# Optimization experiments

Hardware: AMD Instinct MI355X
Metric: run time of the kernel (lower is better)

## Reference

```python
import jax, jax.numpy as jnp
import numpy as np

HID = 1024
HEADS = 16
HEAD_DIM = HID // HEADS
SCALE = HEAD_DIM ** -0.5


def setup_inputs() -> dict:
    key = jax.random.key(0)
    ks = jax.random.split(key, 11)
    B, S = 4, 2048
    std = HID ** -0.5
    inp = {
        'q': jax.random.normal(ks[0], (B, S, HID), jnp.float32),
        'k': jax.random.normal(ks[1], (B, S, HID), jnp.float32),
        'v': jax.random.normal(ks[2], (B, S, HID), jnp.float32),
        'Wq': jax.random.normal(ks[3], (HID, HID), jnp.float32) * std,
        'bq': jnp.zeros((HID,), jnp.float32),
        'Wk': jax.random.normal(ks[4], (HID, HID), jnp.float32) * std,
        'bk': jnp.zeros((HID,), jnp.float32),
        'Wv': jax.random.normal(ks[5], (HID, HID), jnp.float32) * std,
        'bv': jnp.zeros((HID,), jnp.float32),
        'Wo': jax.random.normal(ks[6], (HID, HID), jnp.float32) * std,
        'bo': jnp.zeros((HID,), jnp.float32),
    }
    return inp


def _split_heads(x, B):
    # [B, S, HID] -> [B, H, S, Dh]
    return x.reshape(B, -1, HEADS, HEAD_DIM).transpose(0, 2, 1, 3)


def reference(q, k, v, Wq, bq, Wk, bk, Wv, bv, Wo, bo):
    B = q.shape[0]
    Q = _split_heads(jnp.dot(q, Wq.T) + bq, B)
    K = _split_heads(jnp.dot(k, Wk.T) + bk, B)
    V = _split_heads(jnp.dot(v, Wv.T) + bv, B)
    # [B, H, Sq, Sk]
    energy = jnp.einsum('bhqd,bhkd->bhqk', Q, K) * SCALE
    attention = jax.nn.softmax(energy, axis=-1)
    x = jnp.einsum('bhqk,bhkd->bhqd', attention, V)  # dropout = identity (eval)
    x = x.transpose(0, 2, 1, 3).reshape(B, -1, HID)
    x = jnp.dot(x, Wo.T) + bo
    return (x, attention)
```

## Files before the change

kernel.cpp:

```cpp
#include <hip/hip_runtime.h>
#include <stdint.h>

#define HID 1024
#define HEADS 16
#define HDIM 64
#define SEQ 2048
#define BATCH 4
#define SCALE 0.125f
#define EXPC 0.18033688011112042f

typedef __bf16 bf16x8 __attribute__((ext_vector_type(8)));
typedef float f32x4 __attribute__((ext_vector_type(4)));
typedef unsigned short ushortx8 __attribute__((ext_vector_type(8)));
typedef unsigned short ushortx4 __attribute__((ext_vector_type(4)));

__device__ __forceinline__ unsigned short f2bf(float f) {
  uint32_t u = __builtin_bit_cast(uint32_t, f);
  u = (u + 0x7fffu + ((u >> 16) & 1u)) >> 16;
  return (unsigned short)u;
}
__device__ __forceinline__ float bf2f(unsigned short u) {
  uint32_t x = ((uint32_t)u) << 16;
  return __builtin_bit_cast(float, x);
}
__device__ __forceinline__ void gl16(const void* g, void* l) {
  __builtin_amdgcn_global_load_lds(
      (const __attribute__((address_space(1))) unsigned int*)g,
      (__attribute__((address_space(3))) unsigned int*)l, 16, 0, 0);
}

struct ConvArgs {
  const float* s[7];
  unsigned short* d[7];
  int n[7];
};
__global__ __launch_bounds__(256) void convk(ConvArgs a) {
  const int ten = blockIdx.y;
  const float* s = a.s[ten];
  unsigned short* d = a.d[ten];
  const int n = a.n[ten];
  const int stride = gridDim.x * blockDim.x * 8;
  for (int i = (blockIdx.x * blockDim.x + threadIdx.x) * 8; i < n; i += stride) {
    float4 v0 = *(const float4*)(s + i);
    float4 v1 = *(const float4*)(s + i + 4);
    ushortx8 o = {f2bf(v0.x), f2bf(v0.y), f2bf(v0.z), f2bf(v0.w),
                  f2bf(v1.x), f2bf(v1.y), f2bf(v1.z), f2bf(v1.w)};
    *(ushortx8*)(d + i) = o;
  }
}

struct QkvArgs {
  const unsigned short* A[3];
  const unsigned short* W[3];
  const float* bias[3];
  unsigned short* out[3];
};
__global__ __launch_bounds__(256) void gemm_qkv(QkvArgs ar) {
  __shared__ unsigned short Als[128 * 64];
  __shared__ unsigned short Bls[128 * 64];
  const int z = blockIdx.z;
  const unsigned short* A = ar.A[z];
  const unsigned short* Wb = ar.W[z];
  const float* bias = ar.bias[z];
  unsigned short* Out = ar.out[z];

  const int t = threadIdx.x;
  const int bn = blockIdx.x, bm = blockIdx.y;
  const int w = t >> 6, lane = t & 63;
  const int wm = w >> 1, wn = w & 1;
  const int lr = lane & 15, lk = lane >> 4;
  const int row0 = bm * 128, col0 = bn * 128;

  const unsigned short* Abase =
      A + (size_t)(row0 + w * 32 + (lane >> 3)) * HID + (lane & 7) * 8;
  const unsigned short* Wbase =
      Wb + (size_t)(col0 + w * 32 + (lane >> 3)) * HID + (lane & 7) * 8;

  f32x4 acc[4][4] = {};

  for (int ks = 0; ks < 16; ++ks) {
    __syncthreads();
#pragma unroll
    for (int i = 0; i < 4; ++i)
      gl16(Abase + (size_t)i * 8 * HID + ks * 64, &Als[(w * 32 + i * 8) * 64]);
#pragma unroll
    for (int i = 0; i < 4; ++i)
      gl16(Wbase + (size_t)i * 8 * HID + ks * 64, &Bls[(w * 32 + i * 8) * 64]);
    __syncthreads();
#pragma unroll
    for (int kk = 0; kk < 2; ++kk) {
      bf16x8 a[4], bb[4];
#pragma unroll
      for (int f = 0; f < 4; ++f) {
        a[f] = *(const bf16x8*)&Als[(wm * 64 + f * 16 + lr) * 64 + kk * 32 + lk * 8];
        bb[f] = *(const bf16x8*)&Bls[(wn * 64 + f * 16 + lr) * 64 + kk * 32 + lk * 8];
      }
#pragma unroll
      for (int fm = 0; fm < 4; ++fm)
#pragma unroll
        for (int fn = 0; fn < 4; ++fn)
          acc[fm][fn] = __builtin_amdgcn_mfma_f32_16x16x32_bf16(
              a[fm], bb[fn], acc[fm][fn], 0, 0, 0);
    }
  }

#pragma unroll
  for (int fn = 0; fn < 4; ++fn) {
    int col = col0 + wn * 64 + fn * 16 + lr;
    float bv = bias[col];
#pragma unroll
    for (int fm = 0; fm < 4; ++fm) {
      int row = row0 + wm * 64 + fm * 16 + lk * 4;
      if (z == 2) {
        int b_ = row >> 11, s = row & 2047;
        int hh = col >> 6, d = col & 63;
        ushortx4 o4 = {f2bf(acc[fm][fn][0] + bv), f2bf(acc[fm][fn][1] + bv),
                       f2bf(acc[fm][fn][2] + bv), f2bf(acc[fm][fn][3] + bv)};
        *(ushortx4*)(Out + ((size_t)(b_ * HEADS + hh) * HDIM + d) * SEQ + s) = o4;
      } else {
#pragma unroll
        for (int r = 0; r < 4; ++r)
          Out[(size_t)(row + r) * HID + col] = f2bf(acc[fm][fn][r] + bv);
      }
    }
  }
}

template <int W_F32>
__global__ __launch_bounds__(256) void gemm_wo(
    const unsigned short* __restrict__ A, const void* __restrict__ Wp,
    const float* __restrict__ bias, float* __restrict__ Out) {
  __shared__ unsigned short Als[128 * 64];
  __shared__ unsigned short Bls[128 * 64];
  const int t = threadIdx.x;
  const int bn = blockIdx.x, bm = blockIdx.y;
  const int w = t >> 6, lane = t & 63;
  const int wm = w >> 1, wn = w & 1;
  const int lr = lane & 15, lk = lane >> 4;
  const int row0 = bm * 128, col0 = bn * 128;

  const unsigned short* Abase =
      A + (size_t)(row0 + w * 32 + (lane >> 3)) * HID + (lane & 7) * 8;
  const unsigned short* Wb16 =
      (const unsigned short*)Wp + (size_t)(col0 + w * 32 + (lane >> 3)) * HID +
      (lane & 7) * 8;

  f32x4 acc[4][4] = {};

  for (int ks = 0; ks < 16; ++ks) {
    __syncthreads();
#pragma unroll
    for (int i = 0; i < 4; ++i)
      gl16(Abase + (size_t)i * 8 * HID + ks * 64, &Als[(w * 32 + i * 8) * 64]);
    if (!W_F32) {
#pragma unroll
      for (int i = 0; i < 4; ++i)
        gl16(Wb16 + (size_t)i * 8 * HID + ks * 64, &Bls[(w * 32 + i * 8) * 64]);
    } else {
      const float* Wf = (const float*)Wp;
#pragma unroll
      for (int i = 0; i < 8; ++i) {
        int chunk = t + i * 256;
        int r = chunk >> 4, c4 = (chunk & 15) * 4;
        float4 v4 = *(const float4*)(Wf + (size_t)(col0 + r) * HID + ks * 64 + c4);
        ushortx4 o = {f2bf(v4.x), f2bf(v4.y), f2bf(v4.z), f2bf(v4.w)};
        *(ushortx4*)&Bls[r * 64 + c4] = o;
      }
    }
    __syncthreads();
#pragma unroll
    for (int kk = 0; kk < 2; ++kk) {
      bf16x8 a[4], bb[4];
#pragma unroll
      for (int f = 0; f < 4; ++f) {
        a[f] = *(const bf16x8*)&Als[(wm * 64 + f * 16 + lr) * 64 + kk * 32 + lk * 8];
        bb[f] = *(const bf16x8*)&Bls[(wn * 64 + f * 16 + lr) * 64 + kk * 32 + lk * 8];
      }
#pragma unroll
      for (int fm = 0; fm < 4; ++fm)
#pragma unroll
        for (int fn = 0; fn < 4; ++fn)
          acc[fm][fn] = __builtin_amdgcn_mfma_f32_16x16x32_bf16(
              a[fm], bb[fn], acc[fm][fn], 0, 0, 0);
    }
  }

#pragma unroll
  for (int fn = 0; fn < 4; ++fn) {
    int col = col0 + wn * 64 + fn * 16 + lr;
    float bv = bias[col];
#pragma unroll
    for (int fm = 0; fm < 4; ++fm) {
      int row = row0 + wm * 64 + fm * 16 + lk * 4;
#pragma unroll
      for (int r = 0; r < 4; ++r)
        Out[(size_t)(row + r) * HID + col] = acc[fm][fn][r] + bv;
    }
  }
}

__global__ __launch_bounds__(512) void attn_kern(
    const unsigned short* __restrict__ Qb, const unsigned short* __restrict__ Kb,
    const unsigned short* __restrict__ Vt, float* __restrict__ attn_out,
    unsigned short* __restrict__ Xc) {
  __shared__ unsigned short Qls[128][72];
  __shared__ unsigned short Kls[2][64 * 64];
  __shared__ unsigned short Vls[2][64 * 64];

  const int t = threadIdx.x;
  const int bid = blockIdx.x;
  const int wgid = (bid & 7) * 64 + (bid >> 3);
  const int qbp = wgid & 7;
  const int h = (wgid >> 3) & 15;
  const int b = wgid >> 7;

  const int w = t >> 6, lane = t & 63;
  const int lr = lane & 15, lk = lane >> 4;

  const int srow = lane >> 3;
  const int scol = (lane & 7) ^ srow;
  const unsigned short* gK =
      Kb + ((size_t)b * SEQ + w * 8 + srow) * HID + h * HDIM + scol * 8;
  const unsigned short* gV =
      Vt + ((size_t)(b * HEADS + h) * HDIM + w * 8 + srow) * SEQ + scol * 8;
  unsigned short* lK = &Kls[0][w * 8 * 64];
  unsigned short* lV = &Vls[0][w * 8 * 64];

  for (int qbi = 0; qbi < 2; ++qbi) {
    const int qb = qbp * 2 + qbi;
    const size_t qrow0 = (size_t)b * SEQ + (size_t)qb * 128;

    gl16(gK, lK);
#pragma unroll
    for (int i = 0; i < 2; ++i) {
      int chunk = t + i * 512;
      int r = chunk >> 3, c8 = (chunk & 7) * 8;
      *(ushortx8*)&Qls[r][c8] =
          *(const ushortx8*)(Qb + (qrow0 + r) * HID + h * HDIM + c8);
    }
    __syncthreads();

    bf16x8 qf[2];
#pragma unroll
    for (int kk = 0; kk < 2; ++kk)
      qf[kk] = *(const bf16x8*)&Qls[w * 16 + lr][kk * 32 + lk * 8];
    auto& Pls = Qls;

    float lsum[4] = {0.f, 0.f, 0.f, 0.f};
    int buf = 0;

    for (int kt = 0; kt < 32; ++kt) {
      if (kt < 31) gl16(gK + (size_t)(kt + 1) * 64 * HID, lK + (buf ^ 1) * 4096);
      f32x4 acc[4] = {};
      __builtin_amdgcn_s_setprio(1);
#pragma unroll
      for (int kk = 0; kk < 2; ++kk)
#pragma unroll
        for (int kf = 0; kf < 4; ++kf) {
          bf16x8 bb = *(const bf16x8*)&Kls[buf][(kf * 16 + lr) * 64 +
                                               (((kk * 4 + lk) ^ (lr & 7)) << 3)];
          acc[kf] =
              __builtin_amdgcn_mfma_f32_16x16x32_bf16(qf[kk], bb, acc[kf], 0, 0, 0);
        }
      __builtin_amdgcn_s_setprio(0);
#pragma unroll
      for (int kf = 0; kf < 4; ++kf)
#pragma unroll
        for (int r = 0; r < 4; ++r) lsum[r] += exp2f(acc[kf][r] * EXPC);
      __syncthreads();
      buf ^= 1;
    }

    float invl[4];
#pragma unroll
    for (int r = 0; r < 4; ++r) {
#pragma unroll
      for (int off = 1; off < 16; off <<= 1) lsum[r] += __shfl_xor(lsum[r], off, 64);
      invl[r] = 1.0f / lsum[r];
    }

    f32x4 oacc[4] = {};
    float* attn_base =
        attn_out + ((size_t)(b * HEADS + h) * SEQ + (size_t)qb * 128) * SEQ;

    gl16(gK, lK);
    gl16(gV, lV);
    __syncthreads();
    for (int kt = 0; kt < 32; ++kt) {
      if (kt < 31) {
        gl16(gK + (size_t)(kt + 1) * 64 * HID, lK + (buf ^ 1) * 4096);
        gl16(gV + (size_t)(kt + 1) * 64, lV + (buf ^ 1) * 4096);
      }
      f32x4 acc[4] = {};
      __builtin_amdgcn_s_setprio(1);
#pragma unroll
      for (int kk = 0; kk < 2; ++kk)
#pragma unroll
        for (int kf = 0; kf < 4; ++kf) {
          bf16x8 bb = *(const bf16x8*)&Kls[buf][(kf * 16 + lr) * 64 +
                                               (((kk * 4 + lk) ^ (lr & 7)) << 3)];
          acc[kf] =
              __builtin_amdgcn_mfma_f32_16x16x32_bf16(qf[kk], bb, acc[kf], 0, 0, 0);
        }
      __builtin_amdgcn_s_setprio(0);
#pragma unroll
      for (int kf = 0; kf < 4; ++kf)
#pragma unroll
        for (int r = 0; r < 4; ++r) {
          float p = exp2f(acc[kf][r] * EXPC) * invl[r];
          Pls[w * 16 + lk * 4 + r][kf * 16 + lr] = f2bf(p);
        }
#pragma unroll
      for (int it = 0; it < 4; ++it) {
        int rl = it * 4 + lk;
        ushortx4 p4 = *(const ushortx4*)&Pls[w * 16 + rl][lr * 4];
        f32x4 o = {bf2f(p4[0]), bf2f(p4[1]), bf2f(p4[2]), bf2f(p4[3])};
        __builtin_nontemporal_store(
            o, (f32x4*)(attn_base + (size_t)(w * 16 + rl) * SEQ + kt * 64 + lr * 4));
      }
      __builtin_amdgcn_s_setprio(1);
#pragma unroll
      for (int kk = 0; kk < 2; ++kk) {
        bf16x8 ap = *(const bf16x8*)&Pls[w * 16 + lr][kk * 32 + lk * 8];
#pragma unroll
        for (int df = 0; df < 4; ++df) {
          bf16x8 bv = *(const bf16x8*)&Vls[buf][(df * 16 + lr) * 64 +
                                               (((kk * 4 + lk) ^ (lr & 7)) << 3)];
          oacc[df] = __builtin_amdgcn_mfma_f32_16x16x32_bf16(ap, bv, oacc[df], 0, 0, 0);
        }
      }
      __builtin_amdgcn_s_setprio(0);
      __syncthreads();
      buf ^= 1;
    }

#pragma unroll
    for (int df = 0; df < 4; ++df)
#pragma unroll
      for (int r = 0; r < 4; ++r) {
        int row = w * 16 + lk * 4 + r;
        int col = h * HDIM + df * 16 + lr;
        Xc[(qrow0 + row) * HID + col] = f2bf(oacc[df][r]);
      }
  }
}

extern "C" void kernel_launch(void* const* d_in, const int* in_sizes, int n_in,
                              void* d_out, int out_size, void* d_ws, size_t ws_size,
                              hipStream_t stream) {
  const float* q = (const float*)d_in[0];
  const float* k = (const float*)d_in[1];
  const float* v = (const float*)d_in[2];
  const float* Wq = (const float*)d_in[3];
  const float* bq = (const float*)d_in[4];
  const float* Wk = (const float*)d_in[5];
  const float* bk = (const float*)d_in[6];
  const float* Wv = (const float*)d_in[7];
  const float* bv = (const float*)d_in[8];
  const float* Wo = (const float*)d_in[9];
  const float* bo = (const float*)d_in[10];

  char* ws = (char*)d_ws;
  const size_t MAT = (size_t)8192 * 1024 * sizeof(unsigned short);
  unsigned short* Qbuf = (unsigned short*)(ws);
  unsigned short* Kbuf = (unsigned short*)(ws + MAT);
  unsigned short* Vtb = (unsigned short*)(ws + 2 * MAT);
  unsigned short* Xc = (unsigned short*)(ws + 3 * MAT);

  float* xout = (float*)d_out;
  float* attn_out = xout + (size_t)BATCH * SEQ * HID;

  unsigned short* scr = (unsigned short*)attn_out;
  const int NQ = 8192 * 1024, NW = 1024 * 1024;
  unsigned short* qb16 = scr;
  unsigned short* kb16 = scr + (size_t)NQ;
  unsigned short* vb16 = scr + (size_t)2 * NQ;
  unsigned short* wq16 = scr + (size_t)3 * NQ;
  unsigned short* wk16 = wq16 + NW;
  unsigned short* wv16 = wk16 + NW;
  unsigned short* wo16 = (unsigned short*)(ws + 4 * MAT);
  const bool wo_bf = ws_size >= 4 * MAT + (size_t)NW * sizeof(unsigned short);

  ConvArgs ca;
  ca.s[0] = q;  ca.s[1] = k;  ca.s[2] = v;
  ca.s[3] = Wq; ca.s[4] = Wk; ca.s[5] = Wv; ca.s[6] = Wo;
  ca.d[0] = qb16; ca.d[1] = kb16; ca.d[2] = vb16;
  ca.d[3] = wq16; ca.d[4] = wk16; ca.d[5] = wv16; ca.d[6] = wo16;
  ca.n[0] = NQ; ca.n[1] = NQ; ca.n[2] = NQ;
  ca.n[3] = NW; ca.n[4] = NW; ca.n[5] = NW; ca.n[6] = NW;

  dim3 blk(256);
  hipLaunchKernelGGL(convk, dim3(512, wo_bf ? 7 : 6), blk, 0, stream, ca);

  QkvArgs qa;
  qa.A[0] = qb16; qa.A[1] = kb16; qa.A[2] = vb16;
  qa.W[0] = wq16; qa.W[1] = wk16; qa.W[2] = wv16;
  qa.bias[0] = bq; qa.bias[1] = bk; qa.bias[2] = bv;
  qa.out[0] = Qbuf; qa.out[1] = Kbuf; qa.out[2] = Vtb;
  hipLaunchKernelGGL(gemm_qkv, dim3(8, 64, 3), blk, 0, stream, qa);

  hipLaunchKernelGGL(attn_kern, dim3(512), dim3(512), 0, stream, Qbuf, Kbuf, Vtb,
                     attn_out, Xc);

  dim3 gp(8, 64);
  if (wo_bf)
    hipLaunchKernelGGL((gemm_wo<0>), gp, blk, 0, stream, Xc, wo16, bo, xout);
  else
    hipLaunchKernelGGL((gemm_wo<1>), gp, blk, 0, stream, Xc, Wo, bo, xout);
}
```

Before: 417.7 us.

## Fuse fp32-to-bf16 activation conversion into QKV GEMM and fold softmax scale

The QKV GEMM now reads fp32 q/k/v directly, converting to bf16 while staging into LDS, so the separate conversion pass over the three activation tensors (plus its write and re-read) is dropped. The softmax exp2 scale constant is folded into the Q projection epilogue, which removes a multiply per score in the attention kernel. Both GEMMs also use a 1D grid with an XCD-aware block remap so neighbouring tiles share L2. In exchange, A-tile loads become synchronous register loads instead of async global-to-LDS loads, which may hurt latency hiding in the GEMM.

```diff
diff --git a/kernel.cpp b/kernel.cpp
--- a/kernel.cpp
+++ b/kernel.cpp
@@ -30,9 +30,9 @@
 }
 
 struct ConvArgs {
-  const float* s[7];
-  unsigned short* d[7];
-  int n[7];
+  const float* s[4];
+  unsigned short* d[4];
+  int n[4];
 };
 __global__ __launch_bounds__(256) void convk(ConvArgs a) {
   const int ten = blockIdx.y;
@@ -50,7 +50,7 @@
 }
 
 struct QkvArgs {
-  const unsigned short* A[3];
+  const float* Af[3];
   const unsigned short* W[3];
   const float* bias[3];
   unsigned short* out[3];
@@ -58,21 +58,23 @@
 __global__ __launch_bounds__(256) void gemm_qkv(QkvArgs ar) {
   __shared__ unsigned short Als[128 * 64];
   __shared__ unsigned short Bls[128 * 64];
-  const int z = blockIdx.z;
-  const unsigned short* A = ar.A[z];
+  const int bid = blockIdx.x;
+  const int wgid = (bid & 7) * 192 + (bid >> 3);
+  const int z = wgid >> 9;
+  const int rem = wgid & 511;
+  const int bm = rem >> 3, bn = rem & 7;
+
+  const float* Af = ar.Af[z];
   const unsigned short* Wb = ar.W[z];
   const float* bias = ar.bias[z];
   unsigned short* Out = ar.out[z];
 
   const int t = threadIdx.x;
-  const int bn = blockIdx.x, bm = blockIdx.y;
   const int w = t >> 6, lane = t & 63;
   const int wm = w >> 1, wn = w & 1;
   const int lr = lane & 15, lk = lane >> 4;
   const int row0 = bm * 128, col0 = bn * 128;
 
-  const unsigned short* Abase =
-      A + (size_t)(row0 + w * 32 + (lane >> 3)) * HID + (lane & 7) * 8;
   const unsigned short* Wbase =
       Wb + (size_t)(col0 + w * 32 + (lane >> 3)) * HID + (lane & 7) * 8;
 
@@ -82,10 +84,15 @@
     __syncthreads();
 #pragma unroll
     for (int i = 0; i < 4; ++i)
-      gl16(Abase + (size_t)i * 8 * HID + ks * 64, &Als[(w * 32 + i * 8) * 64]);
-#pragma unroll
-    for (int i = 0; i < 4; ++i)
       gl16(Wbase + (size_t)i * 8 * HID + ks * 64, &Bls[(w * 32 + i * 8) * 64]);
+#pragma unroll
+    for (int i = 0; i < 8; ++i) {
+      int chunk = t + i * 256;
+      int r = chunk >> 4, c4 = (chunk & 15) * 4;
+      float4 v4 = *(const float4*)(Af + (size_t)(row0 + r) * HID + ks * 64 + c4);
+      ushortx4 o = {f2bf(v4.x), f2bf(v4.y), f2bf(v4.z), f2bf(v4.w)};
+      *(ushortx4*)&Als[r * 64 + c4] = o;
+    }
     __syncthreads();
 #pragma unroll
     for (int kk = 0; kk < 2; ++kk) {
@@ -104,6 +111,7 @@
     }
   }
 
+  const float sc = (z == 0) ? EXPC : 1.0f;
 #pragma unroll
   for (int fn = 0; fn < 4; ++fn) {
     int col = col0 + wn * 64 + fn * 16 + lr;
@@ -120,7 +128,7 @@
       } else {
 #pragma unroll
         for (int r = 0; r < 4; ++r)
-          Out[(size_t)(row + r) * HID + col] = f2bf(acc[fm][fn][r] + bv);
+          Out[(size_t)(row + r) * HID + col] = f2bf((acc[fm][fn][r] + bv) * sc);
       }
     }
   }
@@ -132,8 +140,10 @@
     const float* __restrict__ bias, float* __restrict__ Out) {
   __shared__ unsigned short Als[128 * 64];
   __shared__ unsigned short Bls[128 * 64];
+  const int bid = blockIdx.x;
+  const int wgid = (bid & 7) * 64 + (bid >> 3);
+  const int bm = wgid >> 3, bn = wgid & 7;
   const int t = threadIdx.x;
-  const int bn = blockIdx.x, bm = blockIdx.y;
   const int w = t >> 6, lane = t & 63;
   const int wm = w >> 1, wn = w & 1;
   const int lr = lane & 15, lk = lane >> 4;
@@ -266,7 +276,7 @@
 #pragma unroll
       for (int kf = 0; kf < 4; ++kf)
 #pragma unroll
-        for (int r = 0; r < 4; ++r) lsum[r] += exp2f(acc[kf][r] * EXPC);
+        for (int r = 0; r < 4; ++r) lsum[r] += exp2f(acc[kf][r]);
       __syncthreads();
       buf ^= 1;
     }
@@ -307,7 +317,7 @@
       for (int kf = 0; kf < 4; ++kf)
 #pragma unroll
         for (int r = 0; r < 4; ++r) {
-          float p = exp2f(acc[kf][r] * EXPC) * invl[r];
+          float p = exp2f(acc[kf][r]) * invl[r];
           Pls[w * 16 + lk * 4 + r][kf * 16 + lr] = f2bf(p);
         }
 #pragma unroll
@@ -371,40 +381,33 @@
   float* attn_out = xout + (size_t)BATCH * SEQ * HID;
 
   unsigned short* scr = (unsigned short*)attn_out;
-  const int NQ = 8192 * 1024, NW = 1024 * 1024;
-  unsigned short* qb16 = scr;
-  unsigned short* kb16 = scr + (size_t)NQ;
-  unsigned short* vb16 = scr + (size_t)2 * NQ;
-  unsigned short* wq16 = scr + (size_t)3 * NQ;
+  const int NW = 1024 * 1024;
+  unsigned short* wq16 = scr;
   unsigned short* wk16 = wq16 + NW;
   unsigned short* wv16 = wk16 + NW;
   unsigned short* wo16 = (unsigned short*)(ws + 4 * MAT);
   const bool wo_bf = ws_size >= 4 * MAT + (size_t)NW * sizeof(unsigned short);
 
   ConvArgs ca;
-  ca.s[0] = q;  ca.s[1] = k;  ca.s[2] = v;
-  ca.s[3] = Wq; ca.s[4] = Wk; ca.s[5] = Wv; ca.s[6] = Wo;
-  ca.d[0] = qb16; ca.d[1] = kb16; ca.d[2] = vb16;
-  ca.d[3] = wq16; ca.d[4] = wk16; ca.d[5] = wv16; ca.d[6] = wo16;
-  ca.n[0] = NQ; ca.n[1] = NQ; ca.n[2] = NQ;
-  ca.n[3] = NW; ca.n[4] = NW; ca.n[5] = NW; ca.n[6] = NW;
+  ca.s[0] = Wq; ca.s[1] = Wk; ca.s[2] = Wv; ca.s[3] = Wo;
+  ca.d[0] = wq16; ca.d[1] = wk16; ca.d[2] = wv16; ca.d[3] = wo16;
+  ca.n[0] = NW; ca.n[1] = NW; ca.n[2] = NW; ca.n[3] = NW;
 
   dim3 blk(256);
-  hipLaunchKernelGGL(convk, dim3(512, wo_bf ? 7 : 6), blk, 0, stream, ca);
+  hipLaunchKernelGGL(convk, dim3(128, wo_bf ? 4 : 3), blk, 0, stream, ca);
 
   QkvArgs qa;
-  qa.A[0] = qb16; qa.A[1] = kb16; qa.A[2] = vb16;
+  qa.Af[0] = q; qa.Af[1] = k; qa.Af[2] = v;
   qa.W[0] = wq16; qa.W[1] = wk16; qa.W[2] = wv16;
   qa.bias[0] = bq; qa.bias[1] = bk; qa.bias[2] = bv;
   qa.out[0] = Qbuf; qa.out[1] = Kbuf; qa.out[2] = Vtb;
-  hipLaunchKernelGGL(gemm_qkv, dim3(8, 64, 3), blk, 0, stream, qa);
+  hipLaunchKernelGGL(gemm_qkv, dim3(1536), blk, 0, stream, qa);
 
   hipLaunchKernelGGL(attn_kern, dim3(512), dim3(512), 0, stream, Qbuf, Kbuf, Vtb,
                      attn_out, Xc);
 
-  dim3 gp(8, 64);
   if (wo_bf)
-    hipLaunchKernelGGL((gemm_wo<0>), gp, blk, 0, stream, Xc, wo16, bo, xout);
+    hipLaunchKernelGGL((gemm_wo<0>), dim3(512), blk, 0, stream, Xc, wo16, bo, xout);
   else
-    hipLaunchKernelGGL((gemm_wo<1>), gp, blk, 0, stream, Xc, Wo, bo, xout);
-}
+    hipLaunchKernelGGL((gemm_wo<1>), dim3(512), blk, 0, stream, Xc, Wo, bo, xout);
+}
```

After: 401.7 us, median of 3. 1.04x faster.
